# Optimization experiments

Hardware: AMD Instinct MI355X
Metric: run time of the kernel (lower is better)

The kernel has to match this reference:

```python
import jax, jax.numpy as jnp
import numpy as np

C = 64
G = 4          # group_number
K = 3          # kernel_size
R = 4          # reduction_ratio -> bottleneck C//R = 16
BN_EPS = 1e-3  # keras BatchNormalization default epsilon


def setup_inputs() -> dict:
    key = jax.random.key(0)
    ks = jax.random.split(key, 8)
    B, H, W = 8, 192, 192
    cr = C // R
    x = jax.random.normal(ks[0], (B, H, W, C), dtype=jnp.float32)
    # kernel_gen: Conv2D 1x1 (C -> C//R), BN, ReLU, Conv2D 1x1 (C//R -> K*K*G)
    w1 = jax.random.normal(ks[1], (C, cr), dtype=jnp.float32) * (1.0 / np.sqrt(C))
    b1 = jnp.zeros((cr,), dtype=jnp.float32)
    gamma = 1.0 + 0.1 * jax.random.normal(ks[2], (cr,), dtype=jnp.float32)
    beta = 0.1 * jax.random.normal(ks[3], (cr,), dtype=jnp.float32)
    mean = 0.1 * jax.random.normal(ks[4], (cr,), dtype=jnp.float32)
    var = jax.random.uniform(ks[5], (cr,), dtype=jnp.float32, minval=0.5, maxval=1.5)
    w2 = jax.random.normal(ks[6], (cr, K * K * G), dtype=jnp.float32) * (1.0 / np.sqrt(cr))
    b2 = jnp.zeros((K * K * G,), dtype=jnp.float32)
    return {"x": x, "w1": w1, "b1": b1, "gamma": gamma, "beta": beta,
            "mean": mean, "var": var, "w2": w2, "b2": b2}


def reference(x, w1, b1, gamma, beta, mean, var, w2, b2):
    B, H, W, Cc = x.shape
    # --- kernel generation (stride=1 -> identity pooling) ---
    t = jnp.einsum('bhwc,cd->bhwd', x, w1) + b1                 # [B,H,W,C//R]
    t = (t - mean) * jax.lax.rsqrt(var + BN_EPS) * gamma + beta  # BN (inference)
    t = jax.nn.relu(t)
    kern = jnp.einsum('bhwd,de->bhwe', t, w2) + b2               # [B,H,W,K*K*G]
    kern = kern.reshape(B, H, W, K * K, 1, G)
    # --- unfold: tf.image.extract_patches SAME, stride 1, patch order (ki,kj,C) ---
    pad = K // 2
    xp = jnp.pad(x, ((0, 0), (pad, pad), (pad, pad), (0, 0)))
    patches = jnp.stack(
        [xp[:, i:i + H, j:j + W, :] for i in range(K) for j in range(K)],
        axis=3)                                                  # [B,H,W,K*K,C]
    unfolded = patches.reshape(B, H, W, K * K, Cc // G, G)
    # --- per-pixel multiply-reduce over patch axis ---
    out = jnp.sum(kern * unfolded, axis=3)                       # [B,H,W,C//G,G]
    return out.reshape(B, H, W, Cc)
```

## Files before the change

kernel.cpp:

```cpp
#include <hip/hip_runtime.h>


#define B_   8
#define H_   192
#define W_   192
#define CR_  16
#define TH_  8
#define TW_  16
#define TILES_X (W_/TW_)
#define TILES_PER_IMG (TILES_X*(H_/TH_))
#define NBLK (B_*TILES_PER_IMG)
#define NPIX (TH_*TW_)

constexpr float BN_EPS = 1e-3f;

__device__ __forceinline__ float4 mask4(float4 k, bool v) {
    k.x = v ? k.x : 0.f;
    k.y = v ? k.y : 0.f;
    k.z = v ? k.z : 0.f;
    k.w = v ? k.w : 0.f;
    return k;
}

__device__ __forceinline__ void fma4(float4& a, const float4 k, const float4 x) {
    a.x = fmaf(k.x, x.x, a.x);
    a.y = fmaf(k.y, x.y, a.y);
    a.z = fmaf(k.z, x.z, a.z);
    a.w = fmaf(k.w, x.w, a.w);
}

#define LROWS(S, R)                                                         \
    do {                                                                    \
        int rr_ = (R);                                                      \
        if (!INTERIOR) {                                                    \
            if ((unsigned)rr_ < (unsigned)H_) rv |= (1 << (S));             \
            else                              rv &= ~(1 << (S));            \
            rr_ = rr_ < 0 ? 0 : (rr_ >= H_ ? H_ - 1 : rr_);                 \
        }                                                                   \
        const int rb_ = rr_ * (W_ * 16);                                    \
        rgA[S][0] = x4[rb_ + coA[0]];                                       \
        rgA[S][1] = x4[rb_ + coA[1]];                                       \
        rgA[S][2] = x4[rb_ + coA[2]];                                       \
        rgB[S][0] = x4[rb_ + coB[0]];                                       \
        rgB[S][1] = x4[rb_ + coB[1]];                                       \
        rgB[S][2] = x4[rb_ + coB[2]];                                       \
    } while (0)

#define COMP(I)                                                             \
    do {                                                                    \
        const float4* kqA_ = &s_kern[((I) * TW_ + wslot) * 9];              \
        const float4* kqB_ = &s_kern[((I) * TW_ + wslot + 8) * 9];          \
        float4 aA_ = make_float4(0.f, 0.f, 0.f, 0.f);                       \
        float4 aB_ = make_float4(0.f, 0.f, 0.f, 0.f);                       \
        _Pragma("unroll")                                                   \
        for (int ti_ = 0; ti_ < 3; ++ti_) {                                 \
            const int s_ = ((I) + ti_) & 3;                                 \
            _Pragma("unroll")                                               \
            for (int tj_ = 0; tj_ < 3; ++tj_) {                             \
                float4 kA_ = kqA_[ti_ * 3 + tj_];                           \
                float4 kB_ = kqB_[ti_ * 3 + tj_];                           \
                if (!INTERIOR) {                                            \
                    kA_ = mask4(kA_, (((rv >> s_) & (cmA >> tj_)) & 1));    \
                    kB_ = mask4(kB_, (((rv >> s_) & (cmB >> tj_)) & 1));    \
                }                                                           \
                fma4(aA_, kA_, rgA[s_][tj_]);                               \
                fma4(aB_, kB_, rgB[s_][tj_]);                               \
            }                                                               \
        }                                                                   \
        const int ob_ = (th0 + (I)) * (W_ * 16);                            \
        o4[ob_ + (wA << 4) + c4i] = aA_;                                    \
        o4[ob_ + (wB << 4) + c4i] = aB_;                                    \
    } while (0)

#define SFENCE __builtin_amdgcn_sched_barrier(0)

template <bool INTERIOR>
__device__ __forceinline__ void phase_b(const float4* __restrict__ x4,
                                        float4* __restrict__ o4,
                                        const float4* __restrict__ s_kern,
                                        int th0, int tw0, int tid)
{
    const int wslot = tid >> 4;
    const int c4i   = tid & 15;
    const int wA = tw0 + wslot;
    const int wB = tw0 + wslot + 8;

    int coA[3], coB[3];
    int cmA = 7, cmB = 7;
    #pragma unroll
    for (int tj = 0; tj < 3; ++tj) {
        int wa = wA + tj - 1;
        int wb = wB + tj - 1;
        if (!INTERIOR) {
            if ((unsigned)wa >= (unsigned)W_) cmA &= ~(1 << tj);
            if ((unsigned)wb >= (unsigned)W_) cmB &= ~(1 << tj);
            wa = wa < 0 ? 0 : (wa >= W_ ? W_ - 1 : wa);
            wb = wb < 0 ? 0 : (wb >= W_ ? W_ - 1 : wb);
        }
        coA[tj] = (wa << 4) + c4i;
        coB[tj] = (wb << 4) + c4i;
    }

    float4 rgA[4][3], rgB[4][3];
    int rv = 0xF;

    LROWS(0, th0 - 1);
    LROWS(1, th0 + 0);
    LROWS(2, th0 + 1);
    LROWS(3, th0 + 2);
    SFENCE;
    COMP(0); LROWS(0, th0 + 3);
    SFENCE;
    COMP(1); LROWS(1, th0 + 4);
    SFENCE;
    COMP(2); LROWS(2, th0 + 5);
    SFENCE;
    COMP(3); LROWS(3, th0 + 6);
    SFENCE;
    COMP(4); LROWS(0, th0 + 7);
    SFENCE;
    COMP(5); LROWS(1, th0 + 8);
    SFENCE;
    COMP(6);
    COMP(7);
}

#undef LROWS
#undef COMP

__global__ __launch_bounds__(128, 2)
void invol_fused(const float* __restrict__ x,
                 const float* __restrict__ w1,
                 const float* __restrict__ b1,
                 const float* __restrict__ gamma,
                 const float* __restrict__ beta,
                 const float* __restrict__ mean,
                 const float* __restrict__ var,
                 const float* __restrict__ w2,
                 const float* __restrict__ b2,
                 float* __restrict__ out)
{
    __shared__ float4 s_kern[NPIX * 9];

    const int bid = blockIdx.x;
    const int img = bid & 7;
    const int tin = bid >> 3;
    const int th0 = (tin / TILES_X) * TH_;
    const int tw0 = (tin % TILES_X) * TW_;

    const int tid = threadIdx.x;

    {
        const int r = tid >> 4, cc = tid & 15;
        const int h = th0 + r, w = tw0 + cc;
        const float4* xp = reinterpret_cast<const float4*>(
            x + (((size_t)((img * H_ + h) * W_ + w)) << 6));

        float td[CR_];
        #pragma unroll
        for (int d = 0; d < CR_; ++d) td[d] = 0.f;

        #pragma unroll
        for (int c4 = 0; c4 < 16; ++c4) {
            const float4 xv = xp[c4];
            const float xs[4] = {xv.x, xv.y, xv.z, xv.w};
            #pragma unroll
            for (int k = 0; k < 4; ++k) {
                const float* wr = w1 + (c4 * 4 + k) * CR_;
                #pragma unroll
                for (int d = 0; d < CR_; ++d)
                    td[d] = fmaf(xs[k], wr[d], td[d]);
            }
        }

        #pragma unroll
        for (int d = 0; d < CR_; ++d) {
            const float a = gamma[d] * rsqrtf(var[d] + BN_EPS);
            const float c = (b1[d] - mean[d]) * a + beta[d];
            td[d] = fmaxf(fmaf(td[d], a, c), 0.f);
        }

        float ke[36];
        #pragma unroll
        for (int e = 0; e < 36; ++e) ke[e] = b2[e];
        #pragma unroll
        for (int d = 0; d < CR_; ++d) {
            const float t = td[d];
            const float* wr = w2 + d * 36;
            #pragma unroll
            for (int e = 0; e < 36; ++e)
                ke[e] = fmaf(t, wr[e], ke[e]);
        }

        float4* skq = &s_kern[tid * 9];
        #pragma unroll
        for (int t9 = 0; t9 < 9; ++t9)
            skq[t9] = make_float4(ke[t9 * 4 + 0], ke[t9 * 4 + 1],
                                  ke[t9 * 4 + 2], ke[t9 * 4 + 3]);
    }

    __syncthreads();

    const float4* x4 = reinterpret_cast<const float4*>(x) +
                       (size_t)img * (H_ * W_ * 16);
    float4* o4 = reinterpret_cast<float4*>(out) +
                 (size_t)img * (H_ * W_ * 16);

    const bool interior = (th0 > 0) && (th0 + TH_ < H_) &&
                          (tw0 > 0) && (tw0 + TW_ < W_);
    if (interior)
        phase_b<true >(x4, o4, s_kern, th0, tw0, tid);
    else
        phase_b<false>(x4, o4, s_kern, th0, tw0, tid);
}

extern "C" void kernel_launch(void* const* d_in, const int* in_sizes, int n_in,
                              void* d_out, int out_size, void* d_ws, size_t ws_size,
                              hipStream_t stream) {
    const float* x     = (const float*)d_in[0];
    const float* w1    = (const float*)d_in[1];
    const float* b1    = (const float*)d_in[2];
    const float* gamma = (const float*)d_in[3];
    const float* beta  = (const float*)d_in[4];
    const float* mean  = (const float*)d_in[5];
    const float* var   = (const float*)d_in[6];
    const float* w2    = (const float*)d_in[7];
    const float* b2    = (const float*)d_in[8];
    float* out = (float*)d_out;

    invol_fused<<<dim3(NBLK), dim3(128), 0, stream>>>(
        x, w1, b1, gamma, beta, mean, var, w2, b2, out);
}
```

Before: 174.7 us.

## Split fused involution into kernel-generation and apply kernels via workspace

Splits the single fused kernel into two launches. The first generates the per-pixel 36-value kernels for all pixels and writes them to a workspace buffer. The second loads those kernels into shared memory and does the 3x3 multiply-reduce. This separates the register-heavy generation phase from the apply phase, so each kernel can be scheduled with its own occupancy. The cost is an extra ~42 MB write and read of the intermediate kernels plus a second launch. The fused kernel remains as a fallback when no workspace is available.

```diff
diff --git a/kernel.cpp b/kernel.cpp
--- a/kernel.cpp
+++ b/kernel.cpp
@@ -11,6 +11,8 @@
 #define TILES_PER_IMG (TILES_X*(H_/TH_))
 #define NBLK (B_*TILES_PER_IMG)
 #define NPIX (TH_*TW_)
+#define NPIX_TOT (B_*H_*W_)
+#define WS_NEED ((size_t)NPIX_TOT * 36 * 4)
 
 constexpr float BN_EPS = 1e-3f;
 
@@ -27,6 +29,53 @@
     a.y = fmaf(k.y, x.y, a.y);
     a.z = fmaf(k.z, x.z, a.z);
     a.w = fmaf(k.w, x.w, a.w);
+}
+
+__device__ __forceinline__ void kern_math(const float4* __restrict__ xp,
+                                          const float* __restrict__ w1,
+                                          const float* __restrict__ b1,
+                                          const float* __restrict__ gamma,
+                                          const float* __restrict__ beta,
+                                          const float* __restrict__ mean,
+                                          const float* __restrict__ var,
+                                          const float* __restrict__ w2,
+                                          const float* __restrict__ b2,
+                                          float (&ke)[36])
+{
+    float td[CR_];
+    #pragma unroll
+    for (int d = 0; d < CR_; ++d) td[d] = 0.f;
+
+    #pragma unroll
+    for (int c4 = 0; c4 < 16; ++c4) {
+        const float4 xv = xp[c4];
+        const float xs[4] = {xv.x, xv.y, xv.z, xv.w};
+        #pragma unroll
+        for (int k = 0; k < 4; ++k) {
+            const float* wr = w1 + (c4 * 4 + k) * CR_;
+            #pragma unroll
+            for (int d = 0; d < CR_; ++d)
+                td[d] = fmaf(xs[k], wr[d], td[d]);
+        }
+    }
+
+    #pragma unroll
+    for (int d = 0; d < CR_; ++d) {
+        const float a = gamma[d] * rsqrtf(var[d] + BN_EPS);
+        const float c = (b1[d] - mean[d]) * a + beta[d];
+        td[d] = fmaxf(fmaf(td[d], a, c), 0.f);
+    }
+
+    #pragma unroll
+    for (int e = 0; e < 36; ++e) ke[e] = b2[e];
+    #pragma unroll
+    for (int d = 0; d < CR_; ++d) {
+        const float t = td[d];
+        const float* wr = w2 + d * 36;
+        #pragma unroll
+        for (int e = 0; e < 36; ++e)
+            ke[e] = fmaf(t, wr[e], ke[e]);
+    }
 }
 
 #define LROWS(S, R)                                                         \
@@ -128,6 +177,70 @@
 #undef LROWS
 #undef COMP
 
+__global__ __launch_bounds__(256, 2)
+void gen_kern(const float* __restrict__ x,
+              const float* __restrict__ w1,
+              const float* __restrict__ b1,
+              const float* __restrict__ gamma,
+              const float* __restrict__ beta,
+              const float* __restrict__ mean,
+              const float* __restrict__ var,
+              const float* __restrict__ w2,
+              const float* __restrict__ b2,
+              float* __restrict__ ws)
+{
+    const int p = blockIdx.x * 256 + threadIdx.x;
+    const float4* xp = reinterpret_cast<const float4*>(x) + (size_t)p * 16;
+
+    float ke[36];
+    kern_math(xp, w1, b1, gamma, beta, mean, var, w2, b2, ke);
+
+    float4* wp = reinterpret_cast<float4*>(ws) + (size_t)p * 9;
+    #pragma unroll
+    for (int t9 = 0; t9 < 9; ++t9)
+        wp[t9] = make_float4(ke[t9 * 4 + 0], ke[t9 * 4 + 1],
+                             ke[t9 * 4 + 2], ke[t9 * 4 + 3]);
+}
+
+__global__ __launch_bounds__(128, 2)
+void apply_kern(const float* __restrict__ x,
+                const float* __restrict__ ws,
+                float* __restrict__ out)
+{
+    __shared__ float4 s_kern[NPIX * 9];
+
+    const int bid = blockIdx.x;
+    const int img = bid & 7;
+    const int tin = bid >> 3;
+    const int th0 = (tin / TILES_X) * TH_;
+    const int tw0 = (tin % TILES_X) * TW_;
+    const int tid = threadIdx.x;
+
+    {
+        const int r = tid >> 4, cc = tid & 15;
+        const size_t gp = (size_t)((img * H_ + th0 + r) * W_ + (tw0 + cc));
+        const float4* wp = reinterpret_cast<const float4*>(ws) + gp * 9;
+        float4* skq = &s_kern[tid * 9];
+        #pragma unroll
+        for (int t9 = 0; t9 < 9; ++t9)
+            skq[t9] = wp[t9];
+    }
+
+    __syncthreads();
+
+    const float4* x4 = reinterpret_cast<const float4*>(x) +
+                       (size_t)img * (H_ * W_ * 16);
+    float4* o4 = reinterpret_cast<float4*>(out) +
+                 (size_t)img * (H_ * W_ * 16);
+
+    const bool interior = (th0 > 0) && (th0 + TH_ < H_) &&
+                          (tw0 > 0) && (tw0 + TW_ < W_);
+    if (interior)
+        phase_b<true >(x4, o4, s_kern, th0, tw0, tid);
+    else
+        phase_b<false>(x4, o4, s_kern, th0, tw0, tid);
+}
+
 __global__ __launch_bounds__(128, 2)
 void invol_fused(const float* __restrict__ x,
                  const float* __restrict__ w1,
@@ -147,7 +260,6 @@
     const int tin = bid >> 3;
     const int th0 = (tin / TILES_X) * TH_;
     const int tw0 = (tin % TILES_X) * TW_;
-
     const int tid = threadIdx.x;
 
     {
@@ -156,41 +268,8 @@
         const float4* xp = reinterpret_cast<const float4*>(
             x + (((size_t)((img * H_ + h) * W_ + w)) << 6));
 
-        float td[CR_];
-        #pragma unroll
-        for (int d = 0; d < CR_; ++d) td[d] = 0.f;
-
-        #pragma unroll
-        for (int c4 = 0; c4 < 16; ++c4) {
-            const float4 xv = xp[c4];
-            const float xs[4] = {xv.x, xv.y, xv.z, xv.w};
-            #pragma unroll
-            for (int k = 0; k < 4; ++k) {
-                const float* wr = w1 + (c4 * 4 + k) * CR_;
-                #pragma unroll
-                for (int d = 0; d < CR_; ++d)
-                    td[d] = fmaf(xs[k], wr[d], td[d]);
-            }
-        }
-
-        #pragma unroll
-        for (int d = 0; d < CR_; ++d) {
-            const float a = gamma[d] * rsqrtf(var[d] + BN_EPS);
-            const float c = (b1[d] - mean[d]) * a + beta[d];
-            td[d] = fmaxf(fmaf(td[d], a, c), 0.f);
-        }
-
         float ke[36];
-        #pragma unroll
-        for (int e = 0; e < 36; ++e) ke[e] = b2[e];
-        #pragma unroll
-        for (int d = 0; d < CR_; ++d) {
-            const float t = td[d];
-            const float* wr = w2 + d * 36;
-            #pragma unroll
-            for (int e = 0; e < 36; ++e)
-                ke[e] = fmaf(t, wr[e], ke[e]);
-        }
+        kern_math(xp, w1, b1, gamma, beta, mean, var, w2, b2, ke);
 
         float4* skq = &s_kern[tid * 9];
         #pragma unroll
@@ -228,6 +307,13 @@
     const float* b2    = (const float*)d_in[8];
     float* out = (float*)d_out;
 
-    invol_fused<<<dim3(NBLK), dim3(128), 0, stream>>>(
-        x, w1, b1, gamma, beta, mean, var, w2, b2, out);
-}
+    if (d_ws != nullptr && ws_size >= WS_NEED) {
+        float* ws = (float*)d_ws;
+        gen_kern<<<dim3(NPIX_TOT / 256), dim3(256), 0, stream>>>(
+            x, w1, b1, gamma, beta, mean, var, w2, b2, ws);
+        apply_kern<<<dim3(NBLK), dim3(128), 0, stream>>>(x, ws, out);
+    } else {
+        invol_fused<<<dim3(NBLK), dim3(128), 0, stream>>>(
+            x, w1, b1, gamma, beta, mean, var, w2, b2, out);
+    }
+}
```

Result: slower. 187.4 us (+7.3%).

## Assign adjacent column pairs per thread to share halo loads; hoist row prefetch above barrier

Applied to the files above, without the earlier changes.

Each thread now handles two adjacent output columns instead of columns eight apart, so the two 3-wide horizontal windows overlap and need 4 input float4 loads per row instead of 6. This lowers the register footprint for the row ring and the global load count. The __syncthreads after kernel generation moves into phase_b, after the first four rows are issued, so those global loads overlap the barrier wait. Each thread's two stores per row now go to adjacent pixels, which changes the store access pattern.

```diff
diff --git a/kernel.cpp b/kernel.cpp
--- a/kernel.cpp
+++ b/kernel.cpp
@@ -38,18 +38,16 @@
             rr_ = rr_ < 0 ? 0 : (rr_ >= H_ ? H_ - 1 : rr_);                 \
         }                                                                   \
         const int rb_ = rr_ * (W_ * 16);                                    \
-        rgA[S][0] = x4[rb_ + coA[0]];                                       \
-        rgA[S][1] = x4[rb_ + coA[1]];                                       \
-        rgA[S][2] = x4[rb_ + coA[2]];                                       \
-        rgB[S][0] = x4[rb_ + coB[0]];                                       \
-        rgB[S][1] = x4[rb_ + coB[1]];                                       \
-        rgB[S][2] = x4[rb_ + coB[2]];                                       \
+        rg[S][0] = x4[rb_ + co[0]];                                         \
+        rg[S][1] = x4[rb_ + co[1]];                                         \
+        rg[S][2] = x4[rb_ + co[2]];                                         \
+        rg[S][3] = x4[rb_ + co[3]];                                         \
     } while (0)
 
 #define COMP(I)                                                             \
     do {                                                                    \
-        const float4* kqA_ = &s_kern[((I) * TW_ + wslot) * 9];              \
-        const float4* kqB_ = &s_kern[((I) * TW_ + wslot + 8) * 9];          \
+        const float4* kqA_ = &s_kern[((I) * TW_ + 2 * wslot) * 9];          \
+        const float4* kqB_ = kqA_ + 9;                                      \
         float4 aA_ = make_float4(0.f, 0.f, 0.f, 0.f);                       \
         float4 aB_ = make_float4(0.f, 0.f, 0.f, 0.f);                       \
         _Pragma("unroll")                                                   \
@@ -60,16 +58,16 @@
                 float4 kA_ = kqA_[ti_ * 3 + tj_];                           \
                 float4 kB_ = kqB_[ti_ * 3 + tj_];                           \
                 if (!INTERIOR) {                                            \
-                    kA_ = mask4(kA_, (((rv >> s_) & (cmA >> tj_)) & 1));    \
-                    kB_ = mask4(kB_, (((rv >> s_) & (cmB >> tj_)) & 1));    \
+                    kA_ = mask4(kA_, (((rv >> s_) & (cm >> tj_)) & 1));     \
+                    kB_ = mask4(kB_, (((rv >> s_) & (cm >> (tj_ + 1))) & 1));\
                 }                                                           \
-                fma4(aA_, kA_, rgA[s_][tj_]);                               \
-                fma4(aB_, kB_, rgB[s_][tj_]);                               \
+                fma4(aA_, kA_, rg[s_][tj_]);                                \
+                fma4(aB_, kB_, rg[s_][tj_ + 1]);                            \
             }                                                               \
         }                                                                   \
         const int ob_ = (th0 + (I)) * (W_ * 16);                            \
         o4[ob_ + (wA << 4) + c4i] = aA_;                                    \
-        o4[ob_ + (wB << 4) + c4i] = aB_;                                    \
+        o4[ob_ + (wA << 4) + 16 + c4i] = aB_;                               \
     } while (0)
 
 #define SFENCE __builtin_amdgcn_sched_barrier(0)
@@ -82,32 +80,30 @@
 {
     const int wslot = tid >> 4;
     const int c4i   = tid & 15;
-    const int wA = tw0 + wslot;
-    const int wB = tw0 + wslot + 8;
-
-    int coA[3], coB[3];
-    int cmA = 7, cmB = 7;
+    const int wA = tw0 + 2 * wslot;
+
+    int co[4];
+    int cm = 0xF;
     #pragma unroll
-    for (int tj = 0; tj < 3; ++tj) {
-        int wa = wA + tj - 1;
-        int wb = wB + tj - 1;
+    for (int tj = 0; tj < 4; ++tj) {
+        int wc = wA - 1 + tj;
         if (!INTERIOR) {
-            if ((unsigned)wa >= (unsigned)W_) cmA &= ~(1 << tj);
-            if ((unsigned)wb >= (unsigned)W_) cmB &= ~(1 << tj);
-            wa = wa < 0 ? 0 : (wa >= W_ ? W_ - 1 : wa);
-            wb = wb < 0 ? 0 : (wb >= W_ ? W_ - 1 : wb);
-        }
-        coA[tj] = (wa << 4) + c4i;
-        coB[tj] = (wb << 4) + c4i;
+            if ((unsigned)wc >= (unsigned)W_) cm &= ~(1 << tj);
+            wc = wc < 0 ? 0 : (wc >= W_ ? W_ - 1 : wc);
+        }
+        co[tj] = (wc << 4) + c4i;
     }
 
-    float4 rgA[4][3], rgB[4][3];
+    float4 rg[4][4];
     int rv = 0xF;
 
     LROWS(0, th0 - 1);
     LROWS(1, th0 + 0);
     LROWS(2, th0 + 1);
     LROWS(3, th0 + 2);
+
+    __syncthreads();
+
     SFENCE;
     COMP(0); LROWS(0, th0 + 3);
     SFENCE;
@@ -147,7 +143,6 @@
     const int tin = bid >> 3;
     const int th0 = (tin / TILES_X) * TH_;
     const int tw0 = (tin % TILES_X) * TW_;
-
     const int tid = threadIdx.x;
 
     {
@@ -198,8 +193,6 @@
             skq[t9] = make_float4(ke[t9 * 4 + 0], ke[t9 * 4 + 1],
                                   ke[t9 * 4 + 2], ke[t9 * 4 + 3]);
     }
-
-    __syncthreads();
 
     const float4* x4 = reinterpret_cast<const float4*>(x) +
                        (size_t)img * (H_ * W_ * 16);
```

New measurement: 168.9 us. -3.3%, faster.
